# Kernel tuning notes

Measured on AMD Instinct MI355X. Metric: run time of the kernel, lower is better.

## Reference

```python
import jax, jax.numpy as jnp
import numpy as np

NUM_HEADS = 16
THETA = 10000.0


def apply_rope(x, positions, theta=THETA):
    # x: [B, H, S, d_k], positions: [B, S] (broadcast over heads)
    d_k = x.shape[-1]
    inv_freq = theta ** (-jnp.arange(0, d_k // 2, dtype=jnp.float32) * 2.0 / d_k)  # [d_k/2]
    ang = positions[:, None, :, None].astype(jnp.float32) * inv_freq  # [B,1,S,d_k/2]
    cos, sin = jnp.cos(ang), jnp.sin(ang)
    x1 = x[..., 0::2]
    x2 = x[..., 1::2]
    r1 = x1 * cos - x2 * sin
    r2 = x1 * sin + x2 * cos
    # interleave back: [..., d_k/2, 2] -> [..., d_k]
    return jnp.stack([r1, r2], axis=-1).reshape(x.shape)


def setup_inputs() -> dict:
    key = jax.random.key(0)
    ks = jax.random.split(key, 5)
    B, S, D = 1, 4096, 1024
    scale = 1.0 / np.sqrt(D)
    x = jax.random.normal(ks[0], (B, S, D), dtype=jnp.float32)
    Wq = jax.random.normal(ks[1], (D, D), dtype=jnp.float32) * scale
    Wk = jax.random.normal(ks[2], (D, D), dtype=jnp.float32) * scale
    Wv = jax.random.normal(ks[3], (D, D), dtype=jnp.float32) * scale
    Wo = jax.random.normal(ks[4], (D, D), dtype=jnp.float32) * scale
    token_positions = jnp.broadcast_to(jnp.arange(S, dtype=jnp.int32), (B, S))
    return {"x": x, "token_positions": token_positions, "Wq": Wq, "Wk": Wk, "Wv": Wv, "Wo": Wo}


def reference(x, token_positions, Wq, Wk, Wv, Wo):
    B, S, D = x.shape
    H = NUM_HEADS
    d_k = D // H
    # fused QKV projection (Linear: y = x @ W^T, no bias)
    q = jnp.einsum('bsd,ed->bse', x, Wq)
    k = jnp.einsum('bsd,ed->bse', x, Wk)
    v = jnp.einsum('bsd,ed->bse', x, Wv)
    # [B,S,H*dk] -> [B,H,S,dk]
    Q = q.reshape(B, S, H, d_k).transpose(0, 2, 1, 3)
    K = k.reshape(B, S, H, d_k).transpose(0, 2, 1, 3)
    V = v.reshape(B, S, H, d_k).transpose(0, 2, 1, 3)
    Q = apply_rope(Q, token_positions)
    K = apply_rope(K, token_positions)
    scores = jnp.einsum('bhqd,bhkd->bhqk', Q, K) / jnp.sqrt(jnp.float32(d_k))
    causal = jnp.tril(jnp.ones((S, S), dtype=bool))
    scores = jnp.where(causal, scores, -jnp.inf)
    P = jax.nn.softmax(scores, axis=-1)
    out = jnp.einsum('bhqk,bhkd->bhqd', P, V)  # [B,H,S,dk]
    out = out.transpose(0, 2, 1, 3).reshape(B, S, D)
    return jnp.einsum('bsd,ed->bse', out, Wo)
```

## Files before the change

### kernel.cpp

```cpp
#include <hip/hip_runtime.h>
#include <hip/hip_bf16.h>
#include <stdint.h>
#include <math.h>

#define S_LEN   4096
#define D_MODEL 1024
#define NHEAD   16
#define DK      64

typedef __attribute__((ext_vector_type(8))) __bf16 bf16x8;
typedef __attribute__((ext_vector_type(4))) float  f32x4;
using bf16 = __hip_bfloat16;

__device__ __forceinline__ void load_lds16(const bf16* g, bf16* l) {
    __builtin_amdgcn_global_load_lds(
        (const __attribute__((address_space(1))) void*)g,
        (__attribute__((address_space(3))) void*)l, 16, 0, 0);
}

__global__ void cvt_all(const float* __restrict__ x,
                        const float* __restrict__ w0, const float* __restrict__ w1,
                        const float* __restrict__ w2, const float* __restrict__ w3,
                        bf16* __restrict__ xb,
                        bf16* __restrict__ b0, bf16* __restrict__ b1,
                        bf16* __restrict__ b2, bf16* __restrict__ b3)
{
    size_t i4 = ((size_t)blockIdx.x * 256 + threadIdx.x) * 4;
    const float* s; bf16* d; size_t off;
    const size_t NX = (size_t)S_LEN * D_MODEL;
    const size_t NW = (size_t)D_MODEL * D_MODEL;
    if (i4 < NX) { s = x; d = xb; off = i4; }
    else {
        size_t j = i4 - NX;
        int sel = (int)(j >> 20);
        off = j & (NW - 1);
        s = sel == 0 ? w0 : sel == 1 ? w1 : sel == 2 ? w2 : w3;
        d = sel == 0 ? b0 : sel == 1 ? b1 : sel == 2 ? b2 : b3;
    }
    float4 v = *(const float4*)&s[off];
    bf16 t[4] __attribute__((aligned(8)));
    t[0] = __float2bfloat16(v.x); t[1] = __float2bfloat16(v.y);
    t[2] = __float2bfloat16(v.z); t[3] = __float2bfloat16(v.w);
    *(uint64_t*)&d[off] = *(const uint64_t*)t;
}

__global__ __launch_bounds__(256) void qkv_gemm(
    const bf16* __restrict__ Xb,
    const bf16* __restrict__ Wq, const bf16* __restrict__ Wk, const bf16* __restrict__ Wv,
    float* __restrict__ Qf, float* __restrict__ Kf, bf16* __restrict__ VtG)
{
    const int K = D_MODEL, N = D_MODEL;
    int z = blockIdx.z;
    const bf16* B = (z == 0) ? Wq : (z == 1) ? Wk : Wv;

    __shared__ __align__(16) bf16 As[2][128 * 32];
    __shared__ __align__(16) bf16 Bs[2][128 * 32];
    __shared__ __align__(16) bf16 Ts[4][64 * 24];

    int row0 = blockIdx.y * 128;
    int col0 = blockIdx.x * 128;
    int tid  = threadIdx.x;
    int wv   = tid >> 6, lane = tid & 63;
    int m16  = lane & 15, quad = lane >> 4;
    int wr   = (wv >> 1) * 64, wc = (wv & 1) * 64;
    int l4   = lane >> 2, l3 = (lane & 3) * 8;

    const bf16* ga_base = Xb + (size_t)(row0 + wv * 16 + l4) * K + l3;
    const bf16* gb_base = B  + (size_t)(col0 + wv * 16 + l4) * K + l3;

    auto stage = [&](int k0, int buf) {
        load_lds16(ga_base + k0,            &As[buf][wv * 512]);
        load_lds16(ga_base + k0 + 64 * K,   &As[buf][2048 + wv * 512]);
        load_lds16(gb_base + k0,            &Bs[buf][wv * 512]);
        load_lds16(gb_base + k0 + 64 * K,   &Bs[buf][2048 + wv * 512]);
    };

    f32x4 acc[4][4];
    #pragma unroll
    for (int i = 0; i < 4; i++)
        #pragma unroll
        for (int j = 0; j < 4; j++) acc[i][j] = (f32x4){0.f, 0.f, 0.f, 0.f};

    stage(0, 0);
    for (int k0 = 0; k0 < K; k0 += 32) {
        __syncthreads();
        int buf = (k0 >> 5) & 1;
        if (k0 + 32 < K) stage(k0 + 32, buf ^ 1);
        bf16x8 a[4], b[4];
        #pragma unroll
        for (int mi = 0; mi < 4; mi++) a[mi] = *(const bf16x8*)&As[buf][(wr + mi * 16 + m16) * 32 + quad * 8];
        #pragma unroll
        for (int ni = 0; ni < 4; ni++) b[ni] = *(const bf16x8*)&Bs[buf][(wc + ni * 16 + m16) * 32 + quad * 8];
        #pragma unroll
        for (int mi = 0; mi < 4; mi++)
            #pragma unroll
            for (int ni = 0; ni < 4; ni++)
                acc[mi][ni] = __builtin_amdgcn_mfma_f32_16x16x32_bf16(a[mi], b[ni], acc[mi][ni], 0, 0, 0);
    }

    if (z < 2) {
        float* O = (z == 0) ? Qf : Kf;
        #pragma unroll
        for (int mi = 0; mi < 4; mi++)
            #pragma unroll
            for (int ni = 0; ni < 4; ni++)
                #pragma unroll
                for (int r = 0; r < 4; r++) {
                    int gr = row0 + wr + mi * 16 + quad * 4 + r;
                    int gc = col0 + wc + ni * 16 + m16;
                    O[(size_t)gr * N + gc] = acc[mi][ni][r];
                }
    } else {
        #pragma unroll
        for (int mi = 0; mi < 4; mi++) {
            #pragma unroll
            for (int nt = 0; nt < 4; nt++) {
                bf16 t4[4] __attribute__((aligned(8)));
                #pragma unroll
                for (int r = 0; r < 4; r++) t4[r] = __float2bfloat16(acc[mi][nt][r]);
                *(uint64_t*)&Ts[wv][(nt * 16 + m16) * 24 + quad * 4] = *(const uint64_t*)t4;
            }
            #pragma unroll
            for (int rep = 0; rep < 2; rep++) {
                int c  = (lane >> 1) + rep * 32;
                int r8 = lane & 1;
                bf16x8 val = *(const bf16x8*)&Ts[wv][c * 24 + r8 * 8];
                int gc = col0 + wc + c;
                int gr = row0 + wr + mi * 16 + r8 * 8;
                *(bf16x8*)&VtG[(size_t)gc * S_LEN + gr] = val;
            }
        }
    }
}

__global__ __launch_bounds__(256) void out_gemm(
    const bf16* __restrict__ A_, const bf16* __restrict__ B,
    float* __restrict__ C)
{
    const int K = D_MODEL, N = D_MODEL;
    __shared__ __align__(16) bf16 As[2][128 * 32];
    __shared__ __align__(16) bf16 Bs[2][128 * 32];

    int row0 = blockIdx.y * 128;
    int col0 = blockIdx.x * 128;
    int tid  = threadIdx.x;
    int wv   = tid >> 6, lane = tid & 63;
    int m16  = lane & 15, quad = lane >> 4;
    int wr   = (wv >> 1) * 64, wc = (wv & 1) * 64;
    int l4   = lane >> 2, l3 = (lane & 3) * 8;

    const bf16* ga_base = A_ + (size_t)(row0 + wv * 16 + l4) * K + l3;
    const bf16* gb_base = B  + (size_t)(col0 + wv * 16 + l4) * K + l3;

    auto stage = [&](int k0, int buf) {
        load_lds16(ga_base + k0,            &As[buf][wv * 512]);
        load_lds16(ga_base + k0 + 64 * K,   &As[buf][2048 + wv * 512]);
        load_lds16(gb_base + k0,            &Bs[buf][wv * 512]);
        load_lds16(gb_base + k0 + 64 * K,   &Bs[buf][2048 + wv * 512]);
    };

    f32x4 acc[4][4];
    #pragma unroll
    for (int i = 0; i < 4; i++)
        #pragma unroll
        for (int j = 0; j < 4; j++) acc[i][j] = (f32x4){0.f, 0.f, 0.f, 0.f};

    stage(0, 0);
    for (int k0 = 0; k0 < K; k0 += 32) {
        __syncthreads();
        int buf = (k0 >> 5) & 1;
        if (k0 + 32 < K) stage(k0 + 32, buf ^ 1);
        bf16x8 a[4], b[4];
        #pragma unroll
        for (int mi = 0; mi < 4; mi++) a[mi] = *(const bf16x8*)&As[buf][(wr + mi * 16 + m16) * 32 + quad * 8];
        #pragma unroll
        for (int ni = 0; ni < 4; ni++) b[ni] = *(const bf16x8*)&Bs[buf][(wc + ni * 16 + m16) * 32 + quad * 8];
        #pragma unroll
        for (int mi = 0; mi < 4; mi++)
            #pragma unroll
            for (int ni = 0; ni < 4; ni++)
                acc[mi][ni] = __builtin_amdgcn_mfma_f32_16x16x32_bf16(a[mi], b[ni], acc[mi][ni], 0, 0, 0);
    }

    #pragma unroll
    for (int mi = 0; mi < 4; mi++)
        #pragma unroll
        for (int ni = 0; ni < 4; ni++)
            #pragma unroll
            for (int r = 0; r < 4; r++) {
                int gr = row0 + wr + mi * 16 + quad * 4 + r;
                int gc = col0 + wc + ni * 16 + m16;
                C[(size_t)gr * N + gc] = acc[mi][ni][r];
            }
}

__global__ void rope_kernel(const float* __restrict__ Qf, const float* __restrict__ Kf,
                            const int* __restrict__ pos,
                            bf16* __restrict__ Qb, bf16* __restrict__ Kb)
{
    int gid = blockIdx.x * 256 + threadIdx.x;
    size_t i8 = (size_t)gid * 8;
    int s   = (int)(i8 >> 10);
    int col = (int)(i8 & 1023);
    int pair0 = (col & 63) >> 1;
    float p = (float)pos[s];

    float4 qa = *(const float4*)&Qf[i8];
    float4 qb_ = *(const float4*)&Qf[i8 + 4];
    float4 ka = *(const float4*)&Kf[i8];
    float4 kb_ = *(const float4*)&Kf[i8 + 4];
    float q[8] = {qa.x, qa.y, qa.z, qa.w, qb_.x, qb_.y, qb_.z, qb_.w};
    float k[8] = {ka.x, ka.y, ka.z, ka.w, kb_.x, kb_.y, kb_.z, kb_.w};

    bf16 oq[8] __attribute__((aligned(16)));
    bf16 ok[8] __attribute__((aligned(16)));
    const float scale = 0.18033688011112042f;
    #pragma unroll
    for (int j = 0; j < 4; j++) {
        float fi = (float)(pair0 + j);
        float inv = exp2f(fi * (-0.41524101186092028f));
        float ang = p * inv;
        float sn, cs;
        __sincosf(ang, &sn, &cs);
        float q1 = q[2 * j], q2 = q[2 * j + 1];
        float k1 = k[2 * j], k2 = k[2 * j + 1];
        oq[2 * j]     = __float2bfloat16((q1 * cs - q2 * sn) * scale);
        oq[2 * j + 1] = __float2bfloat16((q1 * sn + q2 * cs) * scale);
        ok[2 * j]     = __float2bfloat16(k1 * cs - k2 * sn);
        ok[2 * j + 1] = __float2bfloat16(k1 * sn + k2 * cs);
    }
    *(bf16x8*)&Qb[i8] = *(const bf16x8*)oq;
    *(bf16x8*)&Kb[i8] = *(const bf16x8*)ok;
}

__global__ __launch_bounds__(256, 4) void attn_kernel(
    const bf16* __restrict__ Qb, const bf16* __restrict__ Kb, const bf16* __restrict__ VtG,
    bf16* __restrict__ Attn)
{
    int bx  = blockIdx.x;
    int h   = bx & 15;
    int qt  = 63 - (bx >> 4);
    int tid = threadIdx.x;
    int wv  = tid >> 6, lane = tid & 63;
    int m16 = lane & 15, quad = lane >> 4;
    int csw   = (lane & 3) ^ ((lane >> 3) & 3);
    int colsw = ((quad ^ ((m16 >> 1) & 3)) << 3);
    int psw   = (m16 & 7) ^ ((m16 >> 3) & 1);
    int hc  = h * DK;
    int q0  = qt * 64;

    __shared__ __align__(16) bf16 KT[2][2][64 * 32];
    __shared__ __align__(16) bf16 VT[2][2][64 * 32];
    __shared__ __align__(16) bf16 Ps[64 * 64];

    const bf16* kgl = Kb  + (size_t)(wv * 16 + (lane >> 2)) * D_MODEL + hc + csw * 8;
    const bf16* vgl = VtG + (size_t)(hc + wv * 16 + (lane >> 2)) * S_LEN + csw * 8;

    auto stage = [&](int kb, int buf) {
        size_t ko = (size_t)kb * 64;
        load_lds16(kgl + ko * D_MODEL,       &KT[buf][0][wv * 512]);
        load_lds16(kgl + ko * D_MODEL + 32,  &KT[buf][1][wv * 512]);
        load_lds16(vgl + ko,                 &VT[buf][0][wv * 512]);
        load_lds16(vgl + ko + 32,            &VT[buf][1][wv * 512]);
    };

    const bf16* qp = Qb + (size_t)(q0 + wv * 16 + m16) * D_MODEL + hc;
    bf16x8 aq0 = *(const bf16x8*)&qp[quad * 8];
    bf16x8 aq1 = *(const bf16x8*)&qp[32 + quad * 8];

    bf16x8 bone;
    #pragma unroll
    for (int j = 0; j < 8; j++) bone[j] = (__bf16)1.0f;

    f32x4 o[4];
    f32x4 o_sum = (f32x4){0.f, 0.f, 0.f, 0.f};
    #pragma unroll
    for (int dt = 0; dt < 4; dt++) o[dt] = (f32x4){0.f, 0.f, 0.f, 0.f};

    const float SHIFT = 8.0f;
    const int myq = q0 + wv * 16 + m16;
    const int psrow = (wv * 16 + m16) * 64;

    stage(0, 0);
    for (int kb = 0; kb <= qt; ++kb) {
        __syncthreads();
        int buf = kb & 1;
        if (kb < qt) stage(kb + 1, buf ^ 1);
        int kbase = kb * 64;
        bool diag = (kb == qt);

        #pragma unroll
        for (int nt = 0; nt < 4; nt++) {
            bf16x8 k0 = *(const bf16x8*)&KT[buf][0][(nt * 16 + m16) * 32 + colsw];
            bf16x8 k1 = *(const bf16x8*)&KT[buf][1][(nt * 16 + m16) * 32 + colsw];
            f32x4 zv = (f32x4){0.f, 0.f, 0.f, 0.f};
            zv = __builtin_amdgcn_mfma_f32_16x16x32_bf16(k0, aq0, zv, 0, 0, 0);
            zv = __builtin_amdgcn_mfma_f32_16x16x32_bf16(k1, aq1, zv, 0, 0, 0);

            bf16 t4[4] __attribute__((aligned(8)));
            #pragma unroll
            for (int r = 0; r < 4; r++) {
                float pv = __builtin_amdgcn_exp2f(zv[r] - SHIFT);
                if (diag) {
                    int key = kbase + nt * 16 + quad * 4 + r;
                    if (key > myq) pv = 0.f;
                }
                t4[r] = __float2bfloat16(pv);
            }
            int cw = (nt * 2 + (quad >> 1)) ^ psw;
            *(uint64_t*)&Ps[psrow + cw * 8 + (quad & 1) * 4] = *(const uint64_t*)t4;
        }

        int c0 = quad ^ psw;
        bf16x8 ap0 = *(const bf16x8*)&Ps[psrow + c0 * 8];
        bf16x8 ap1 = *(const bf16x8*)&Ps[psrow + (c0 ^ 4) * 8];

        #pragma unroll
        for (int dt = 0; dt < 4; dt++) {
            bf16x8 v0 = *(const bf16x8*)&VT[buf][0][(dt * 16 + m16) * 32 + colsw];
            bf16x8 v1 = *(const bf16x8*)&VT[buf][1][(dt * 16 + m16) * 32 + colsw];
            o[dt] = __builtin_amdgcn_mfma_f32_16x16x32_bf16(ap0, v0, o[dt], 0, 0, 0);
            o[dt] = __builtin_amdgcn_mfma_f32_16x16x32_bf16(ap1, v1, o[dt], 0, 0, 0);
        }
        o_sum = __builtin_amdgcn_mfma_f32_16x16x32_bf16(ap0, bone, o_sum, 0, 0, 0);
        o_sum = __builtin_amdgcn_mfma_f32_16x16x32_bf16(ap1, bone, o_sum, 0, 0, 0);
    }

    #pragma unroll
    for (int r = 0; r < 4; r++) {
        float inv = 1.0f / o_sum[r];
        int rowg = q0 + wv * 16 + quad * 4 + r;
        #pragma unroll
        for (int dt = 0; dt < 4; dt++)
            Attn[(size_t)rowg * D_MODEL + hc + dt * 16 + m16] =
                __float2bfloat16(o[dt][r] * inv);
    }
}

extern "C" void kernel_launch(void* const* d_in, const int* in_sizes, int n_in,
                              void* d_out, int out_size, void* d_ws, size_t ws_size,
                              hipStream_t stream)
{
    const float* x  = (const float*)d_in[0];
    const int*   pos= (const int*)d_in[1];
    const float* Wq = (const float*)d_in[2];
    const float* Wk = (const float*)d_in[3];
    const float* Wv = (const float*)d_in[4];
    const float* Wo = (const float*)d_in[5];
    float* out = (float*)d_out;

    char* ws = (char*)d_ws;
    bf16*  xb   = (bf16*) (ws);
    bf16*  wqb  = (bf16*) (ws + ( 8ull << 20));
    bf16*  wkb  = (bf16*) (ws + (10ull << 20));
    bf16*  wvb  = (bf16*) (ws + (12ull << 20));
    bf16*  wob  = (bf16*) (ws + (14ull << 20));
    float* Qf   = (float*)(ws + (16ull << 20));
    float* Kf   = (float*)(ws + (32ull << 20));
    bf16*  Qb   = (bf16*) (ws + (48ull << 20));
    bf16*  Kb   = (bf16*) (ws + (56ull << 20));
    bf16*  VtG  = (bf16*) (ws + (64ull << 20));
    bf16*  Attn = (bf16*) (ws + (72ull << 20));

    cvt_all<<<8192, 256, 0, stream>>>(x, Wq, Wk, Wv, Wo, xb, wqb, wkb, wvb, wob);

    qkv_gemm<<<dim3(8, 32, 3), 256, 0, stream>>>(xb, wqb, wkb, wvb, Qf, Kf, VtG);

    rope_kernel<<<2048, 256, 0, stream>>>(Qf, Kf, pos, Qb, Kb);

    attn_kernel<<<dim3(1024), 256, 0, stream>>>(Qb, Kb, VtG, Attn);

    out_gemm<<<dim3(8, 32), 256, 0, stream>>>(Attn, wob, out);
}
```

Before: 214.8 us.

## Fuse RoPE into QKV GEMM epilogue and shrink out-projection tile width

Applies RoPE and the Q scaling directly in the QKV GEMM epilogue, using a lane shuffle to pair even and odd columns, and writes bf16 Q/K straight out. This removes the fp32 Q/K intermediates and the separate rope kernel launch along with its global memory traffic. The output GEMM tile is also narrowed from 128 to 64 columns, doubling its grid to 512 blocks for better CU occupancy at the cost of more A-tile reloads. The epilogue now does sincos per element inside the GEMM, which adds ALU work and register pressure there.

```diff
diff --git a/kernel.cpp b/kernel.cpp
--- a/kernel.cpp
+++ b/kernel.cpp
@@ -47,7 +47,8 @@
 __global__ __launch_bounds__(256) void qkv_gemm(
     const bf16* __restrict__ Xb,
     const bf16* __restrict__ Wq, const bf16* __restrict__ Wk, const bf16* __restrict__ Wv,
-    float* __restrict__ Qf, float* __restrict__ Kf, bf16* __restrict__ VtG)
+    const int* __restrict__ pos,
+    bf16* __restrict__ Qb, bf16* __restrict__ Kb, bf16* __restrict__ VtG)
 {
     const int K = D_MODEL, N = D_MODEL;
     int z = blockIdx.z;
@@ -99,17 +100,35 @@
     }
 
     if (z < 2) {
-        float* O = (z == 0) ? Qf : Kf;
-        #pragma unroll
-        for (int mi = 0; mi < 4; mi++)
-            #pragma unroll
-            for (int ni = 0; ni < 4; ni++)
+        bf16* O = (z == 0) ? Qb : Kb;
+        const float qscale = (z == 0) ? 0.18033688011112042f : 1.0f;
+        float invf[4];
+        #pragma unroll
+        for (int ni = 0; ni < 4; ni++) {
+            float fi = (float)((ni * 16 + m16) >> 1);
+            invf[ni] = exp2f(fi * (-0.41524101186092028f));
+        }
+        bool odd = (m16 & 1) != 0;
+        #pragma unroll
+        for (int mi = 0; mi < 4; mi++) {
+            #pragma unroll
+            for (int r = 0; r < 4; r++) {
+                int gr = row0 + wr + mi * 16 + quad * 4 + r;
+                float p = (float)pos[gr];
                 #pragma unroll
-                for (int r = 0; r < 4; r++) {
-                    int gr = row0 + wr + mi * 16 + quad * 4 + r;
+                for (int ni = 0; ni < 4; ni++) {
+                    float own   = acc[mi][ni][r];
+                    float other = __shfl_xor(own, 1);
+                    float sn, cs;
+                    __sincosf(p * invf[ni], &sn, &cs);
+                    float x1 = odd ? other : own;
+                    float x2 = odd ? own   : other;
+                    float res = odd ? (x1 * sn + x2 * cs) : (x1 * cs - x2 * sn);
                     int gc = col0 + wc + ni * 16 + m16;
-                    O[(size_t)gr * N + gc] = acc[mi][ni][r];
+                    O[(size_t)gr * N + gc] = __float2bfloat16(res * qscale);
                 }
+            }
+        }
     } else {
         #pragma unroll
         for (int mi = 0; mi < 4; mi++) {
@@ -139,14 +158,14 @@
 {
     const int K = D_MODEL, N = D_MODEL;
     __shared__ __align__(16) bf16 As[2][128 * 32];
-    __shared__ __align__(16) bf16 Bs[2][128 * 32];
+    __shared__ __align__(16) bf16 Bs[2][64 * 32];
 
     int row0 = blockIdx.y * 128;
-    int col0 = blockIdx.x * 128;
+    int col0 = blockIdx.x * 64;
     int tid  = threadIdx.x;
     int wv   = tid >> 6, lane = tid & 63;
     int m16  = lane & 15, quad = lane >> 4;
-    int wr   = (wv >> 1) * 64, wc = (wv & 1) * 64;
+    int wr   = (wv >> 1) * 64, wc = (wv & 1) * 32;
     int l4   = lane >> 2, l3 = (lane & 3) * 8;
 
     const bf16* ga_base = A_ + (size_t)(row0 + wv * 16 + l4) * K + l3;
@@ -156,81 +175,41 @@
         load_lds16(ga_base + k0,            &As[buf][wv * 512]);
         load_lds16(ga_base + k0 + 64 * K,   &As[buf][2048 + wv * 512]);
         load_lds16(gb_base + k0,            &Bs[buf][wv * 512]);
-        load_lds16(gb_base + k0 + 64 * K,   &Bs[buf][2048 + wv * 512]);
     };
 
-    f32x4 acc[4][4];
+    f32x4 acc[4][2];
     #pragma unroll
     for (int i = 0; i < 4; i++)
         #pragma unroll
-        for (int j = 0; j < 4; j++) acc[i][j] = (f32x4){0.f, 0.f, 0.f, 0.f};
+        for (int j = 0; j < 2; j++) acc[i][j] = (f32x4){0.f, 0.f, 0.f, 0.f};
 
     stage(0, 0);
     for (int k0 = 0; k0 < K; k0 += 32) {
         __syncthreads();
         int buf = (k0 >> 5) & 1;
         if (k0 + 32 < K) stage(k0 + 32, buf ^ 1);
-        bf16x8 a[4], b[4];
+        bf16x8 a[4], b[2];
         #pragma unroll
         for (int mi = 0; mi < 4; mi++) a[mi] = *(const bf16x8*)&As[buf][(wr + mi * 16 + m16) * 32 + quad * 8];
         #pragma unroll
-        for (int ni = 0; ni < 4; ni++) b[ni] = *(const bf16x8*)&Bs[buf][(wc + ni * 16 + m16) * 32 + quad * 8];
+        for (int ni = 0; ni < 2; ni++) b[ni] = *(const bf16x8*)&Bs[buf][(wc + ni * 16 + m16) * 32 + quad * 8];
         #pragma unroll
         for (int mi = 0; mi < 4; mi++)
             #pragma unroll
-            for (int ni = 0; ni < 4; ni++)
+            for (int ni = 0; ni < 2; ni++)
                 acc[mi][ni] = __builtin_amdgcn_mfma_f32_16x16x32_bf16(a[mi], b[ni], acc[mi][ni], 0, 0, 0);
     }
 
     #pragma unroll
     for (int mi = 0; mi < 4; mi++)
         #pragma unroll
-        for (int ni = 0; ni < 4; ni++)
+        for (int ni = 0; ni < 2; ni++)
             #pragma unroll
             for (int r = 0; r < 4; r++) {
                 int gr = row0 + wr + mi * 16 + quad * 4 + r;
                 int gc = col0 + wc + ni * 16 + m16;
                 C[(size_t)gr * N + gc] = acc[mi][ni][r];
             }
-}
-
-__global__ void rope_kernel(const float* __restrict__ Qf, const float* __restrict__ Kf,
-                            const int* __restrict__ pos,
-                            bf16* __restrict__ Qb, bf16* __restrict__ Kb)
-{
-    int gid = blockIdx.x * 256 + threadIdx.x;
-    size_t i8 = (size_t)gid * 8;
-    int s   = (int)(i8 >> 10);
-    int col = (int)(i8 & 1023);
-    int pair0 = (col & 63) >> 1;
-    float p = (float)pos[s];
-
-    float4 qa = *(const float4*)&Qf[i8];
-    float4 qb_ = *(const float4*)&Qf[i8 + 4];
-    float4 ka = *(const float4*)&Kf[i8];
-    float4 kb_ = *(const float4*)&Kf[i8 + 4];
-    float q[8] = {qa.x, qa.y, qa.z, qa.w, qb_.x, qb_.y, qb_.z, qb_.w};
-    float k[8] = {ka.x, ka.y, ka.z, ka.w, kb_.x, kb_.y, kb_.z, kb_.w};
-
-    bf16 oq[8] __attribute__((aligned(16)));
-    bf16 ok[8] __attribute__((aligned(16)));
-    const float scale = 0.18033688011112042f;
-    #pragma unroll
-    for (int j = 0; j < 4; j++) {
-        float fi = (float)(pair0 + j);
-        float inv = exp2f(fi * (-0.41524101186092028f));
-        float ang = p * inv;
-        float sn, cs;
-        __sincosf(ang, &sn, &cs);
-        float q1 = q[2 * j], q2 = q[2 * j + 1];
-        float k1 = k[2 * j], k2 = k[2 * j + 1];
-        oq[2 * j]     = __float2bfloat16((q1 * cs - q2 * sn) * scale);
-        oq[2 * j + 1] = __float2bfloat16((q1 * sn + q2 * cs) * scale);
-        ok[2 * j]     = __float2bfloat16(k1 * cs - k2 * sn);
-        ok[2 * j + 1] = __float2bfloat16(k1 * sn + k2 * cs);
-    }
-    *(bf16x8*)&Qb[i8] = *(const bf16x8*)oq;
-    *(bf16x8*)&Kb[i8] = *(const bf16x8*)ok;
 }
 
 __global__ __launch_bounds__(256, 4) void attn_kernel(
@@ -355,20 +334,16 @@
     bf16*  wkb  = (bf16*) (ws + (10ull << 20));
     bf16*  wvb  = (bf16*) (ws + (12ull << 20));
     bf16*  wob  = (bf16*) (ws + (14ull << 20));
-    float* Qf   = (float*)(ws + (16ull << 20));
-    float* Kf   = (float*)(ws + (32ull << 20));
-    bf16*  Qb   = (bf16*) (ws + (48ull << 20));
-    bf16*  Kb   = (bf16*) (ws + (56ull << 20));
-    bf16*  VtG  = (bf16*) (ws + (64ull << 20));
-    bf16*  Attn = (bf16*) (ws + (72ull << 20));
+    bf16*  Qb   = (bf16*) (ws + (16ull << 20));
+    bf16*  Kb   = (bf16*) (ws + (24ull << 20));
+    bf16*  VtG  = (bf16*) (ws + (32ull << 20));
+    bf16*  Attn = (bf16*) (ws + (40ull << 20));
 
     cvt_all<<<8192, 256, 0, stream>>>(x, Wq, Wk, Wv, Wo, xb, wqb, wkb, wvb, wob);
 
-    qkv_gemm<<<dim3(8, 32, 3), 256, 0, stream>>>(xb, wqb, wkb, wvb, Qf, Kf, VtG);
-
-    rope_kernel<<<2048, 256, 0, stream>>>(Qf, Kf, pos, Qb, Kb);
+    qkv_gemm<<<dim3(8, 32, 3), 256, 0, stream>>>(xb, wqb, wkb, wvb, pos, Qb, Kb, VtG);
 
     attn_kernel<<<dim3(1024), 256, 0, stream>>>(Qb, Kb, VtG, Attn);
 
-    out_gemm<<<dim3(8, 32), 256, 0, stream>>>(Attn, wob, out);
-}
+    out_gemm<<<dim3(16, 32), 256, 0, stream>>>(Attn, wob, out);
+}
```

New measurement: 210.9 us. No clear change (-1.8%).
